# Kernel tuning notes

Hardware: AMD Instinct MI355X
Metric: run time of the kernel (lower is better)

## Reference

```python
import jax, jax.numpy as jnp
import numpy as np

N, E, G = 100_000, 1_200_000, 256
EPS = 1e-5

def _bn(a, g, b):
    # BatchNorm1d in training mode: biased batch statistics over dim 0
    mu = a.mean(0)
    var = ((a - mu) ** 2).mean(0)
    return (a - mu) * jax.lax.rsqrt(var + EPS) * g + b

def _cgconv(x, src, dst, ea, Wf, bf, Ws, bs, g, b):
    # PyG CGConv: z = [x_i, x_j, edge_attr]; m = sigmoid(lin_f(z)) * softplus(lin_s(z));
    # out = BN(scatter_add(m -> dst)) + x
    z = jnp.concatenate([x[dst], x[src], ea], axis=-1)      # [E, 2*64+1]
    m = jax.nn.sigmoid(z @ Wf + bf) * jax.nn.softplus(z @ Ws + bs)  # [E, 64]
    agg = jax.ops.segment_sum(m, dst, num_segments=x.shape[0])
    return _bn(agg, g, b) + x

def setup_inputs() -> dict:
    key = jax.random.key(0)
    ks = jax.random.split(key, 16)
    def w(k, shape, scale):
        return jax.random.normal(k, shape, jnp.float32) * scale
    inp = {
        "x": jax.random.normal(ks[0], (N, 12), jnp.float32),
        "edge_index": jax.random.randint(ks[1], (2, E), 0, N, jnp.int32),
        "edge_attr": jax.random.uniform(ks[2], (E, 1), dtype=jnp.float32),
        "batch": jnp.sort(jax.random.randint(ks[3], (N,), 0, G, jnp.int32)),
        "W_in": w(ks[4], (12, 64), 0.3), "b_in": jnp.zeros((64,), jnp.float32),
        "g0": jnp.ones((64,), jnp.float32), "beta0": jnp.zeros((64,), jnp.float32),
    }
    i = 5
    for l in (1, 2, 3):
        inp[f"Wf{l}"] = w(ks[i], (129, 64), 0.1)
        inp[f"bf{l}"] = jnp.zeros((64,), jnp.float32)
        inp[f"Ws{l}"] = w(ks[i + 1], (129, 64), 0.1)
        inp[f"bs{l}"] = jnp.zeros((64,), jnp.float32)
        inp[f"g{l}"] = jnp.ones((64,), jnp.float32)
        inp[f"bb{l}"] = jnp.zeros((64,), jnp.float32)
        i += 2
    inp["W1"] = w(ks[11], (64, 32), 0.15)
    inp["b1"] = jnp.zeros((32,), jnp.float32)
    inp["W2"] = w(ks[12], (32, 1), 0.2)
    inp["b2"] = jnp.zeros((1,), jnp.float32)
    return inp

def reference(x, edge_index, edge_attr, batch,
              W_in, b_in, g0, beta0,
              Wf1, bf1, Ws1, bs1, g1, bb1,
              Wf2, bf2, Ws2, bs2, g2, bb2,
              Wf3, bf3, Ws3, bs3, g3, bb3,
              W1, b1, W2, b2):
    src, dst = edge_index[0], edge_index[1]
    h = jax.nn.relu(_bn(x @ W_in + b_in, g0, beta0))
    h = jax.nn.relu(_cgconv(h, src, dst, edge_attr, Wf1, bf1, Ws1, bs1, g1, bb1))
    h = jax.nn.relu(_cgconv(h, src, dst, edge_attr, Wf2, bf2, Ws2, bs2, g2, bb2))
    h = _cgconv(h, src, dst, edge_attr, Wf3, bf3, Ws3, bs3, g3, bb3)
    # global_mean_pool
    s = jax.ops.segment_sum(h, batch, num_segments=G)
    c = jax.ops.segment_sum(jnp.ones((h.shape[0],), h.dtype), batch, num_segments=G)
    pooled = s / jnp.maximum(c, 1.0)[:, None]
    return jax.nn.relu(pooled @ W1 + b1) @ W2 + b2  # [G, 1]
```

## Files before the change

kernel.cpp:

```cpp
#include <hip/hip_runtime.h>
#include <math.h>

#define N_NODES 100000
#define N_EDGES 1200000
#define N_GRAPHS 256
#define CH 64
#define NC (N_NODES * CH)
#define EPS 1e-5f
#define LOG2E 1.4426950408889634f
#define LN2 0.6931471805599453f
#define EA_SCALE 32768.0f

#define ZSTRN 72
#define GTILES ((N_NODES + 63) / 64)
#define EA_BLOCKS 4096
#define NW (EA_BLOCKS * 4)
#define POOL_BLOCKS 256
#define WP2ROWS 64
#define CAP 48
#define LDSQ 1024

#define NCOLORS 8
#define SC_BLOCKS 2048
#define NCHUNK (SC_BLOCKS / NCOLORS)
#define CSZ ((N_EDGES + NCHUNK - 1) / NCHUNK)
#define RNODES ((N_NODES + NCOLORS - 1) / NCOLORS)

#define EMB_BLOCKS 512
#define PREP_BLOCKS 192
#define PRE_BLOCKS (SC_BLOCKS + EMB_BLOCKS + PREP_BLOCKS)

typedef _Float16 half8 __attribute__((ext_vector_type(8)));
typedef _Float16 half2v __attribute__((ext_vector_type(2)));
typedef float floatx4 __attribute__((ext_vector_type(4)));

__device__ __forceinline__ float gate2(float f2, float s2) {
    float ef = __builtin_amdgcn_exp2f(-f2);
    float sig = __builtin_amdgcn_rcpf(1.0f + ef);
    float es = __builtin_amdgcn_exp2f(-fabsf(s2));
    float sp = fmaxf(s2, 0.0f) + __builtin_amdgcn_logf(1.0f + es);
    return sig * sp;
}

__global__ void pre_kernel(const int* __restrict__ ei,
                           const float* __restrict__ ea,
                           int* __restrict__ cnt,
                           unsigned* __restrict__ sef2,
                           const float* __restrict__ x,
                           const float* __restrict__ W,
                           const float* __restrict__ b,
                           _Float16* __restrict__ emb,
                           float* __restrict__ stats,
                           const float* __restrict__ Wf0, const float* __restrict__ Ws0,
                           const float* __restrict__ bf0, const float* __restrict__ bs0,
                           const float* __restrict__ Wf1, const float* __restrict__ Ws1,
                           const float* __restrict__ bf1, const float* __restrict__ bs1,
                           const float* __restrict__ Wf2, const float* __restrict__ Ws2,
                           const float* __restrict__ bf2, const float* __restrict__ bs2,
                           _Float16* __restrict__ WT2,
                           float* __restrict__ w128,
                           float* __restrict__ bias) {
    __shared__ int lcnt;
    __shared__ int ldst[LDSQ];
    __shared__ unsigned lpay[LDSQ];
    const int bid = blockIdx.x;
    if (bid < SC_BLOCKS) {
        if (threadIdx.x == 0) lcnt = 0;
        __syncthreads();
        const int j = bid & (NCOLORS - 1);
        const int k = bid >> 3;
        const int dlo = j * RNODES;
        const int dhi = min(N_NODES, dlo + RNODES);
        const int e0 = k * CSZ;
        const int e1 = min(N_EDGES, e0 + CSZ);
        for (int e = e0 + threadIdx.x; e < e1; e += 256) {
            int d = ei[N_EDGES + e];
            if (d >= dlo && d < dhi) {
                unsigned v = ((unsigned)ei[e] << 15) | (unsigned)(ea[e] * EA_SCALE);
                int i = atomicAdd(&lcnt, 1);
                if (i < LDSQ) { ldst[i] = d; lpay[i] = v; }
                else {
                    int slot = atomicAdd(&cnt[d], 1);
                    if (slot < CAP) sef2[(size_t)d * CAP + slot] = v;
                }
            }
        }
        __syncthreads();
        const int m = min(lcnt, LDSQ);
        for (int i = threadIdx.x; i < m; i += 256) {
            int d = ldst[i];
            int slot = atomicAdd(&cnt[d], 1);
            if (slot < CAP) sef2[(size_t)d * CAP + slot] = lpay[i];
        }
    } else if (bid < SC_BLOCKS + EMB_BLOCKS) {
        const int eb = bid - SC_BLOCKS;
        int c = threadIdx.x & 63;
        int sub = threadIdx.x >> 6;
        float s = 0.f, q = 0.f;
        for (int r = eb * 4 + sub; r < N_NODES; r += EMB_BLOCKS * 4) {
            const float* xr = x + r * 12;
            float acc = b[c];
#pragma unroll
            for (int k = 0; k < 12; ++k)
                acc = fmaf(xr[k], W[k * CH + c], acc);
            _Float16 h = (_Float16)acc;
            emb[(size_t)r * CH + c] = h;
            float hf = (float)h;
            s += hf;
            q = fmaf(hf, hf, q);
        }
        __shared__ float ls[4][64];
        __shared__ float lq[4][64];
        ls[sub][c] = s;
        lq[sub][c] = q;
        __syncthreads();
        if (sub == 0) {
            s = ls[0][c] + ls[1][c] + ls[2][c] + ls[3][c];
            q = lq[0][c] + lq[1][c] + lq[2][c] + lq[3][c];
            atomicAdd(&stats[c], s);
            atomicAdd(&stats[64 + c], q);
        }
    } else {
        int gid = (bid - SC_BLOCKS - EMB_BLOCKS) * 256 + threadIdx.x;
        int l = gid >> 14;
        int idx = gid & 16383;
        if (l >= 3) return;
        const float* Wf = (l == 0) ? Wf0 : (l == 1) ? Wf1 : Wf2;
        const float* Ws = (l == 0) ? Ws0 : (l == 1) ? Ws1 : Ws2;
        const float* bf = (l == 0) ? bf0 : (l == 1) ? bf1 : bf2;
        const float* bs = (l == 0) ? bs0 : (l == 1) ? bs1 : bs2;
        {
            int cc = idx >> 6;
            int k = idx & 63;
            float v;
            if (cc < 128) {
                int ch = cc >> 1;
                v = (cc & 1) ? Ws[k * 64 + ch] : Wf[k * 64 + ch];
            } else {
                int jj = cc - 128, ch = jj >> 1;
                v = (jj & 1) ? Ws[(64 + k) * 64 + ch] : Wf[(64 + k) * 64 + ch];
            }
            WT2[l * 16384 + idx] = (_Float16)(v * LOG2E);
        }
        if (idx < 128) {
            w128[l * 128 + idx] = ((idx < 64) ? Wf[128 * 64 + idx] : Ws[128 * 64 + (idx - 64)])
                                  * (LOG2E / EA_SCALE);
            bias[l * 128 + idx] = ((idx < 64) ? bf[idx] : bs[idx - 64]) * LOG2E;
        }
    }
}

template <bool RES, bool RED>
__global__ __launch_bounds__(256)
void node_gemm_kernel(const _Float16* __restrict__ ain,
                      const _Float16* __restrict__ res,
                      const float* __restrict__ stats,
                      const float* __restrict__ gamma,
                      const float* __restrict__ beta,
                      const _Float16* __restrict__ WT2,
                      _Float16* __restrict__ hout,
                      _Float16* __restrict__ pqrs) {
    __shared__ __align__(16) _Float16 As[64 * ZSTRN];
    __shared__ __align__(16) float ab[128];
    __shared__ float sw[128];
    const int t = threadIdx.x;
    const int lane = t & 63;
    const int w = t >> 6;
    const int l15 = lane & 15;
    const int quad = lane >> 4;

    if (RED) {
        if (t < 128) {
            float s = 0.f;
#pragma unroll 8
            for (int r = 0; r < WP2ROWS; ++r) s += stats[r * 128 + t];
            sw[t] = s;
        }
        __syncthreads();
    }
    if (t < 64) {
        float s0 = RED ? sw[t] : stats[t];
        float s1 = RED ? sw[64 + t] : stats[64 + t];
        float mean = s0 * (1.0f / (float)N_NODES);
        float var  = s1 * (1.0f / (float)N_NODES) - mean * mean;
        float inv  = rsqrtf(var + EPS);
        float A = gamma[t] * inv;
        ab[t] = A;
        ab[64 + t] = beta[t] - mean * A;
    }

    half8 bfr[4][2];
#pragma unroll
    for (int tt = 0; tt < 4; ++tt)
#pragma unroll
        for (int ks = 0; ks < 2; ++ks)
            bfr[tt][ks] = *(const half8*)(WT2 + (w * 64 + tt * 16 + l15) * 64 + ks * 32 + quad * 8);
    __syncthreads();

    const int base = blockIdx.x * 64;
    {
        const int e = t >> 2, q = t & 3;
        const int row = base + e;
        const bool valid = (row < N_NODES);
        const int crow = valid ? row : (N_NODES - 1);
        float af[16];
        {
            const _Float16* aph = ain + (size_t)crow * CH + q * 16;
            half8 h0 = *(const half8*)aph;
            half8 h1 = *(const half8*)(aph + 8);
#pragma unroll
            for (int j = 0; j < 8; ++j) { af[j] = (float)h0[j]; af[8 + j] = (float)h1[j]; }
        }
        float rf[16];
        if (RES) {
            const _Float16* rph = res + (size_t)crow * CH + q * 16;
            half8 r0 = *(const half8*)rph;
            half8 r1 = *(const half8*)(rph + 8);
#pragma unroll
            for (int j = 0; j < 8; ++j) { rf[j] = (float)r0[j]; rf[8 + j] = (float)r1[j]; }
        }
        float vv[16];
#pragma unroll
        for (int i = 0; i < 4; ++i) {
            float4 A4 = *(const float4*)(ab + q * 16 + i * 4);
            float4 B4 = *(const float4*)(ab + 64 + q * 16 + i * 4);
#pragma unroll
            for (int jj = 0; jj < 4; ++jj) {
                float Ax = (jj == 0) ? A4.x : (jj == 1) ? A4.y : (jj == 2) ? A4.z : A4.w;
                float Bx = (jj == 0) ? B4.x : (jj == 1) ? B4.y : (jj == 2) ? B4.z : B4.w;
                float r = RES ? rf[i * 4 + jj] : 0.f;
                vv[i * 4 + jj] = fmaxf(fmaf(af[i * 4 + jj], Ax, Bx) + r, 0.0f);
            }
        }
        half8 o0, o1;
#pragma unroll
        for (int j = 0; j < 8; ++j) { o0[j] = (_Float16)vv[j]; o1[j] = (_Float16)vv[8 + j]; }
        *(half8*)(As + e * ZSTRN + q * 16) = o0;
        *(half8*)(As + e * ZSTRN + q * 16 + 8) = o1;
        if (valid) {
            half8* hp = (half8*)(hout + (size_t)row * CH + q * 16);
            hp[0] = o0;
            hp[1] = o1;
        }
    }
    __syncthreads();

    floatx4 acc[4][4];
#pragma unroll
    for (int rt = 0; rt < 4; ++rt)
#pragma unroll
        for (int tt = 0; tt < 4; ++tt)
#pragma unroll
            for (int r = 0; r < 4; ++r) acc[rt][tt][r] = 0.f;

#pragma unroll
    for (int ks = 0; ks < 2; ++ks) {
#pragma unroll
        for (int rt = 0; rt < 4; ++rt) {
            half8 a = *(const half8*)(As + (rt * 16 + l15) * ZSTRN + ks * 32 + quad * 8);
#pragma unroll
            for (int tt = 0; tt < 4; ++tt)
                acc[rt][tt] = __builtin_amdgcn_mfma_f32_16x16x32_f16(a, bfr[tt][ks], acc[rt][tt], 0, 0, 0);
        }
    }

#pragma unroll
    for (int rt = 0; rt < 4; ++rt) {
#pragma unroll
        for (int r = 0; r < 4; ++r) {
            int row = base + rt * 16 + quad * 4 + r;
            if (row < N_NODES) {
#pragma unroll
                for (int tt = 0; tt < 4; ++tt)
                    pqrs[(size_t)row * 256 + w * 64 + tt * 16 + l15] = (_Float16)acc[rt][tt][r];
            }
        }
    }
}

__global__ __launch_bounds__(256)
void edge_agg_kernel(const _Float16* __restrict__ pqrs,
                     const unsigned* __restrict__ sef2,
                     const int* __restrict__ cnt,
                     const float* __restrict__ w128,
                     const float* __restrict__ bias,
                     _Float16* __restrict__ agg,
                     float* __restrict__ wpart2) {
    const int lane = threadIdx.x & 63;
    const int w = threadIdx.x >> 6;
    const int gw = __builtin_amdgcn_readfirstlane(blockIdx.x * 4 + w);
    const float wfc = w128[lane], wsc = w128[64 + lane];
    const float bfc = bias[lane], bsc = bias[64 + lane];
    const half2v* __restrict__ prb = (const half2v*)pqrs;
    const half2v* __restrict__ qsb = (const half2v*)pqrs + 64;

    const int n0 = (int)((long)gw * N_NODES / NW);
    const int n1 = (int)((long)(gw + 1) * N_NODES / NW);

    float ssum = 0.f, sqsum = 0.f;
    if (n0 < n1) {
        half2v prn = prb[(size_t)n0 * 128 + lane];
        for (int n = n0; n < n1; ++n) {
            int deg = cnt[n];
            if (deg > CAP) deg = CAP;
            const unsigned* sp = sef2 + (size_t)n * CAP;
            half2v pr = prn;
            {
                int np = (n + 1 < N_NODES) ? (n + 1) : (N_NODES - 1);
                prn = prb[(size_t)np * 128 + lane];
            }
            const float fb = (float)pr[0] + bfc;
            const float sb = (float)pr[1] + bsc;
            float acc0 = 0.f, acc1 = 0.f, acc2 = 0.f, acc3 = 0.f;
            int e = 0;
            for (; e + 8 <= deg; e += 8) {
                unsigned s0 = sp[e],     s1 = sp[e + 1], s2 = sp[e + 2], s3 = sp[e + 3];
                unsigned s4 = sp[e + 4], s5 = sp[e + 5], s6 = sp[e + 6], s7 = sp[e + 7];
                half2v q0 = qsb[(size_t)(s0 >> 15) * 128 + lane];
                half2v q1 = qsb[(size_t)(s1 >> 15) * 128 + lane];
                half2v q2 = qsb[(size_t)(s2 >> 15) * 128 + lane];
                half2v q3 = qsb[(size_t)(s3 >> 15) * 128 + lane];
                half2v q4 = qsb[(size_t)(s4 >> 15) * 128 + lane];
                half2v q5 = qsb[(size_t)(s5 >> 15) * 128 + lane];
                half2v q6 = qsb[(size_t)(s6 >> 15) * 128 + lane];
                half2v q7 = qsb[(size_t)(s7 >> 15) * 128 + lane];
                float ea0 = (float)(s0 & 32767u), ea1 = (float)(s1 & 32767u);
                float ea2 = (float)(s2 & 32767u), ea3 = (float)(s3 & 32767u);
                float ea4 = (float)(s4 & 32767u), ea5 = (float)(s5 & 32767u);
                float ea6 = (float)(s6 & 32767u), ea7 = (float)(s7 & 32767u);
                acc0 += gate2(fmaf(ea0, wfc, fb + (float)q0[0]), fmaf(ea0, wsc, sb + (float)q0[1]));
                acc1 += gate2(fmaf(ea1, wfc, fb + (float)q1[0]), fmaf(ea1, wsc, sb + (float)q1[1]));
                acc2 += gate2(fmaf(ea2, wfc, fb + (float)q2[0]), fmaf(ea2, wsc, sb + (float)q2[1]));
                acc3 += gate2(fmaf(ea3, wfc, fb + (float)q3[0]), fmaf(ea3, wsc, sb + (float)q3[1]));
                acc0 += gate2(fmaf(ea4, wfc, fb + (float)q4[0]), fmaf(ea4, wsc, sb + (float)q4[1]));
                acc1 += gate2(fmaf(ea5, wfc, fb + (float)q5[0]), fmaf(ea5, wsc, sb + (float)q5[1]));
                acc2 += gate2(fmaf(ea6, wfc, fb + (float)q6[0]), fmaf(ea6, wsc, sb + (float)q6[1]));
                acc3 += gate2(fmaf(ea7, wfc, fb + (float)q7[0]), fmaf(ea7, wsc, sb + (float)q7[1]));
            }
            if (e + 4 <= deg) {
                unsigned s0 = sp[e], s1 = sp[e + 1], s2 = sp[e + 2], s3 = sp[e + 3];
                half2v q0 = qsb[(size_t)(s0 >> 15) * 128 + lane];
                half2v q1 = qsb[(size_t)(s1 >> 15) * 128 + lane];
                half2v q2 = qsb[(size_t)(s2 >> 15) * 128 + lane];
                half2v q3 = qsb[(size_t)(s3 >> 15) * 128 + lane];
                float ea0 = (float)(s0 & 32767u), ea1 = (float)(s1 & 32767u);
                float ea2 = (float)(s2 & 32767u), ea3 = (float)(s3 & 32767u);
                acc0 += gate2(fmaf(ea0, wfc, fb + (float)q0[0]), fmaf(ea0, wsc, sb + (float)q0[1]));
                acc1 += gate2(fmaf(ea1, wfc, fb + (float)q1[0]), fmaf(ea1, wsc, sb + (float)q1[1]));
                acc2 += gate2(fmaf(ea2, wfc, fb + (float)q2[0]), fmaf(ea2, wsc, sb + (float)q2[1]));
                acc3 += gate2(fmaf(ea3, wfc, fb + (float)q3[0]), fmaf(ea3, wsc, sb + (float)q3[1]));
                e += 4;
            }
            for (; e < deg; ++e) {
                unsigned s0 = sp[e];
                half2v q0 = qsb[(size_t)(s0 >> 15) * 128 + lane];
                float ea0 = (float)(s0 & 32767u);
                acc0 += gate2(fmaf(ea0, wfc, fb + (float)q0[0]), fmaf(ea0, wsc, sb + (float)q0[1]));
            }
            _Float16 ah = (_Float16)(LN2 * ((acc0 + acc1) + (acc2 + acc3)));
            agg[(size_t)n * CH + lane] = ah;
            float acc = (float)ah;
            ssum += acc;
            sqsum = fmaf(acc, acc, sqsum);
        }
    }
    __shared__ float reds[4][128];
    reds[w][lane] = ssum;
    reds[w][64 + lane] = sqsum;
    __syncthreads();
    if (w == 0) {
        float a = reds[0][lane] + reds[1][lane] + reds[2][lane] + reds[3][lane];
        float b = reds[0][64 + lane] + reds[1][64 + lane] + reds[2][64 + lane] + reds[3][64 + lane];
        float* wp = wpart2 + (size_t)(blockIdx.x & (WP2ROWS - 1)) * 128;
        atomicAdd(&wp[lane], a);
        atomicAdd(&wp[64 + lane], b);
    }
}

__global__ __launch_bounds__(256)
void pool_bn_kernel(const _Float16* __restrict__ ain,
                    const _Float16* __restrict__ res,
                    const float* __restrict__ wp2,
                    const float* __restrict__ gamma,
                    const float* __restrict__ beta,
                    const int* __restrict__ batch,
                    float* __restrict__ pooled,
                    float* __restrict__ counts) {
    __shared__ float sw[128];
    __shared__ float ab[128];
    if (threadIdx.x < 128) {
        float s = 0.f;
#pragma unroll 8
        for (int r = 0; r < WP2ROWS; ++r) s += wp2[r * 128 + threadIdx.x];
        sw[threadIdx.x] = s;
    }
    __syncthreads();
    if (threadIdx.x < 64) {
        int t = threadIdx.x;
        float mean = sw[t] * (1.0f / (float)N_NODES);
        float var  = sw[64 + t] * (1.0f / (float)N_NODES) - mean * mean;
        float inv  = rsqrtf(var + EPS);
        float A = gamma[t] * inv;
        ab[t] = A;
        ab[64 + t] = beta[t] - mean * A;
    }
    __syncthreads();

    const int c = threadIdx.x & 63;
    const float A = ab[c], B = ab[64 + c];
    const int walker = blockIdx.x * 4 + (threadIdx.x >> 6);
    const int nwalk = POOL_BLOCKS * 4;
    const int chunk = (N_NODES + nwalk - 1) / nwalk;
    int r0 = walker * chunk;
    int r1 = min(N_NODES, r0 + chunk);
    if (r0 >= r1) return;

    int cur = batch[r0];
    float acc = 0.0f;
    int runlen = 0;
    for (int r = r0; r < r1; ++r) {
        int b = batch[r];
        if (b != cur) {
            atomicAdd(&pooled[cur * CH + c], acc);
            if (c == 0) atomicAdd(&counts[cur], (float)runlen);
            acc = 0.0f;
            runlen = 0;
            cur = b;
        }
        size_t idx = (size_t)r * CH + c;
        acc += fmaf((float)ain[idx], A, B) + (float)res[idx];
        ++runlen;
    }
    atomicAdd(&pooled[cur * CH + c], acc);
    if (c == 0) atomicAdd(&counts[cur], (float)runlen);
}

__global__ void head_kernel(const float* __restrict__ pooled,
                            const float* __restrict__ counts,
                            const float* __restrict__ W1,
                            const float* __restrict__ b1,
                            const float* __restrict__ W2,
                            const float* __restrict__ b2,
                            float* __restrict__ out) {
    int gph = blockIdx.x;
    int t = threadIdx.x;
    __shared__ float p[64];
    __shared__ float h1[32];
    float cnt = fmaxf(counts[gph], 1.0f);
    p[t] = pooled[gph * CH + t] / cnt;
    __syncthreads();
    if (t < 32) {
        float acc = b1[t];
#pragma unroll
        for (int c = 0; c < 64; ++c)
            acc = fmaf(p[c], W1[c * 32 + t], acc);
        h1[t] = fmaxf(acc, 0.0f);
    }
    __syncthreads();
    if (t == 0) {
        float acc = b2[0];
#pragma unroll
        for (int j = 0; j < 32; ++j)
            acc = fmaf(h1[j], W2[j], acc);
        out[gph] = acc;
    }
}

extern "C" void kernel_launch(void* const* d_in, const int* in_sizes, int n_in,
                              void* d_out, int out_size, void* d_ws, size_t ws_size,
                              hipStream_t stream) {
    const float* x     = (const float*)d_in[0];
    const int*   ei    = (const int*)d_in[1];
    const float* ea    = (const float*)d_in[2];
    const int*   batch = (const int*)d_in[3];
    const float* W_in  = (const float*)d_in[4];
    const float* b_in  = (const float*)d_in[5];
    const float* g0    = (const float*)d_in[6];
    const float* beta0 = (const float*)d_in[7];

    const float* Wf[3] = {(const float*)d_in[8],  (const float*)d_in[14], (const float*)d_in[20]};
    const float* bfv[3]= {(const float*)d_in[9],  (const float*)d_in[15], (const float*)d_in[21]};
    const float* Wsv[3]= {(const float*)d_in[10], (const float*)d_in[16], (const float*)d_in[22]};
    const float* bsv[3]= {(const float*)d_in[11], (const float*)d_in[17], (const float*)d_in[23]};
    const float* gm[3] = {(const float*)d_in[12], (const float*)d_in[18], (const float*)d_in[24]};
    const float* bb[3] = {(const float*)d_in[13], (const float*)d_in[19], (const float*)d_in[25]};

    const float* W1 = (const float*)d_in[26];
    const float* b1 = (const float*)d_in[27];
    const float* W2 = (const float*)d_in[28];
    const float* b2 = (const float*)d_in[29];

    float* out = (float*)d_out;

#define ALIGN256(v) (((v) + 255) & ~(size_t)255)
    char* base = (char*)d_ws;
    size_t off = 0;
    _Float16* bufA = (_Float16*)(base + off); off = ALIGN256(off + (size_t)NC * 2);
    _Float16* bufB = (_Float16*)(base + off); off = ALIGN256(off + (size_t)NC * 2);
    _Float16* AGG = (_Float16*)(base + off);  off = ALIGN256(off + (size_t)NC * 2);
    _Float16* WT2 = (_Float16*)(base + off);  off = ALIGN256(off + 3 * 256 * 64 * 2);
    float* w128   = (float*)(base + off);     off = ALIGN256(off + 3 * 128 * 4);
    float* biasL  = (float*)(base + off);     off = ALIGN256(off + 3 * 128 * 4);
    unsigned* sef2 = (unsigned*)(base + off); off = ALIGN256(off + (size_t)N_NODES * CAP * 4);
    _Float16* pqrs = (_Float16*)(base + off); off = ALIGN256(off + (size_t)N_NODES * 256 * 2);
    char* zbase   = base + off;
    int* cnt      = (int*)(base + off);       off = ALIGN256(off + (size_t)N_NODES * 4);
    float* stats0 = (float*)(base + off);     off = ALIGN256(off + 128 * 4);
    float* wpart2 = (float*)(base + off);     off = ALIGN256(off + 3 * WP2ROWS * 128 * 4);
    float* pooled = (float*)(base + off);     off = ALIGN256(off + (size_t)N_GRAPHS * CH * 4);
    float* counts = (float*)(base + off);     off = ALIGN256(off + (size_t)N_GRAPHS * 4);
    size_t zbytes = (size_t)(base + off - zbase);

    hipMemsetAsync(zbase, 0, zbytes, stream);

    pre_kernel<<<PRE_BLOCKS, 256, 0, stream>>>(
        ei, ea, cnt, sef2, x, W_in, b_in, bufA, stats0,
        Wf[0], Wsv[0], bfv[0], bsv[0],
        Wf[1], Wsv[1], bfv[1], bsv[1],
        Wf[2], Wsv[2], bfv[2], bsv[2],
        WT2, w128, biasL);

    node_gemm_kernel<false, false><<<GTILES, 256, 0, stream>>>(
        bufA, nullptr, stats0, g0, beta0, WT2 + 0 * 256 * 64, bufB, pqrs);
    edge_agg_kernel<<<EA_BLOCKS, 256, 0, stream>>>(
        pqrs, sef2, cnt, w128 + 0 * 128, biasL + 0 * 128, AGG,
        wpart2 + 0 * WP2ROWS * 128);

    node_gemm_kernel<true, true><<<GTILES, 256, 0, stream>>>(
        AGG, bufB, wpart2 + 0 * WP2ROWS * 128, gm[0], bb[0], WT2 + 1 * 256 * 64, bufA, pqrs);
    edge_agg_kernel<<<EA_BLOCKS, 256, 0, stream>>>(
        pqrs, sef2, cnt, w128 + 1 * 128, biasL + 1 * 128, AGG,
        wpart2 + 1 * WP2ROWS * 128);

    node_gemm_kernel<true, true><<<GTILES, 256, 0, stream>>>(
        AGG, bufA, wpart2 + 1 * WP2ROWS * 128, gm[1], bb[1], WT2 + 2 * 256 * 64, bufB, pqrs);
    edge_agg_kernel<<<EA_BLOCKS, 256, 0, stream>>>(
        pqrs, sef2, cnt, w128 + 2 * 128, biasL + 2 * 128, AGG,
        wpart2 + 2 * WP2ROWS * 128);

    pool_bn_kernel<<<POOL_BLOCKS, 256, 0, stream>>>(
        AGG, bufB, wpart2 + 2 * WP2ROWS * 128, gm[2], bb[2], batch, pooled, counts);
    head_kernel<<<N_GRAPHS, 64, 0, stream>>>(pooled, counts, W1, b1, W2, b2, out);
}
```

Baseline: 499.0 us.

## Move edge scatter into first node GEMM kernel to overlap with GEMM

The edge bucketing scatter (building per-destination edge lists) moves out of the pre kernel and into a new combined kernel. There its blocks are interleaved with the first-layer node GEMM tiles, so the memory- and atomic-bound scatter runs alongside the MFMA-bound GEMM. The pre kernel now only does the embedding and weight preparation, so it is shorter and the GEMM no longer waits for the scatter. The trade-off is higher LDS use per block in the combined kernel, which may lower occupancy for the GEMM blocks.

```diff
diff --git a/kernel.cpp b/kernel.cpp
--- a/kernel.cpp
+++ b/kernel.cpp
@@ -28,7 +28,12 @@
 
 #define EMB_BLOCKS 512
 #define PREP_BLOCKS 192
-#define PRE_BLOCKS (SC_BLOCKS + EMB_BLOCKS + PREP_BLOCKS)
+#define PRE2_BLOCKS (EMB_BLOCKS + PREP_BLOCKS)
+
+#define GS_GROUPS 196
+#define GS_ILV (GS_GROUPS * 16)
+#define GS_SCAT_ILV (GS_GROUPS * 8)
+#define GS_BLOCKS (GS_ILV + (SC_BLOCKS - GS_SCAT_ILV))
 
 typedef _Float16 half8 __attribute__((ext_vector_type(8)));
 typedef _Float16 half2v __attribute__((ext_vector_type(2)));
@@ -42,62 +47,26 @@
     return sig * sp;
 }
 
-__global__ void pre_kernel(const int* __restrict__ ei,
-                           const float* __restrict__ ea,
-                           int* __restrict__ cnt,
-                           unsigned* __restrict__ sef2,
-                           const float* __restrict__ x,
-                           const float* __restrict__ W,
-                           const float* __restrict__ b,
-                           _Float16* __restrict__ emb,
-                           float* __restrict__ stats,
-                           const float* __restrict__ Wf0, const float* __restrict__ Ws0,
-                           const float* __restrict__ bf0, const float* __restrict__ bs0,
-                           const float* __restrict__ Wf1, const float* __restrict__ Ws1,
-                           const float* __restrict__ bf1, const float* __restrict__ bs1,
-                           const float* __restrict__ Wf2, const float* __restrict__ Ws2,
-                           const float* __restrict__ bf2, const float* __restrict__ bs2,
-                           _Float16* __restrict__ WT2,
-                           float* __restrict__ w128,
-                           float* __restrict__ bias) {
-    __shared__ int lcnt;
-    __shared__ int ldst[LDSQ];
-    __shared__ unsigned lpay[LDSQ];
+__global__ void pre2_kernel(const float* __restrict__ x,
+                            const float* __restrict__ W,
+                            const float* __restrict__ b,
+                            _Float16* __restrict__ emb,
+                            float* __restrict__ stats,
+                            const float* __restrict__ Wf0, const float* __restrict__ Ws0,
+                            const float* __restrict__ bf0, const float* __restrict__ bs0,
+                            const float* __restrict__ Wf1, const float* __restrict__ Ws1,
+                            const float* __restrict__ bf1, const float* __restrict__ bs1,
+                            const float* __restrict__ Wf2, const float* __restrict__ Ws2,
+                            const float* __restrict__ bf2, const float* __restrict__ bs2,
+                            _Float16* __restrict__ WT2,
+                            float* __restrict__ w128,
+                            float* __restrict__ bias) {
     const int bid = blockIdx.x;
-    if (bid < SC_BLOCKS) {
-        if (threadIdx.x == 0) lcnt = 0;
-        __syncthreads();
-        const int j = bid & (NCOLORS - 1);
-        const int k = bid >> 3;
-        const int dlo = j * RNODES;
-        const int dhi = min(N_NODES, dlo + RNODES);
-        const int e0 = k * CSZ;
-        const int e1 = min(N_EDGES, e0 + CSZ);
-        for (int e = e0 + threadIdx.x; e < e1; e += 256) {
-            int d = ei[N_EDGES + e];
-            if (d >= dlo && d < dhi) {
-                unsigned v = ((unsigned)ei[e] << 15) | (unsigned)(ea[e] * EA_SCALE);
-                int i = atomicAdd(&lcnt, 1);
-                if (i < LDSQ) { ldst[i] = d; lpay[i] = v; }
-                else {
-                    int slot = atomicAdd(&cnt[d], 1);
-                    if (slot < CAP) sef2[(size_t)d * CAP + slot] = v;
-                }
-            }
-        }
-        __syncthreads();
-        const int m = min(lcnt, LDSQ);
-        for (int i = threadIdx.x; i < m; i += 256) {
-            int d = ldst[i];
-            int slot = atomicAdd(&cnt[d], 1);
-            if (slot < CAP) sef2[(size_t)d * CAP + slot] = lpay[i];
-        }
-    } else if (bid < SC_BLOCKS + EMB_BLOCKS) {
-        const int eb = bid - SC_BLOCKS;
+    if (bid < EMB_BLOCKS) {
         int c = threadIdx.x & 63;
         int sub = threadIdx.x >> 6;
         float s = 0.f, q = 0.f;
-        for (int r = eb * 4 + sub; r < N_NODES; r += EMB_BLOCKS * 4) {
+        for (int r = bid * 4 + sub; r < N_NODES; r += EMB_BLOCKS * 4) {
             const float* xr = x + r * 12;
             float acc = b[c];
 #pragma unroll
@@ -121,7 +90,7 @@
             atomicAdd(&stats[64 + c], q);
         }
     } else {
-        int gid = (bid - SC_BLOCKS - EMB_BLOCKS) * 256 + threadIdx.x;
+        int gid = (bid - EMB_BLOCKS) * 256 + threadIdx.x;
         int l = gid >> 14;
         int idx = gid & 16383;
         if (l >= 3) return;
@@ -146,6 +115,160 @@
             w128[l * 128 + idx] = ((idx < 64) ? Wf[128 * 64 + idx] : Ws[128 * 64 + (idx - 64)])
                                   * (LOG2E / EA_SCALE);
             bias[l * 128 + idx] = ((idx < 64) ? bf[idx] : bs[idx - 64]) * LOG2E;
+        }
+    }
+}
+
+__global__ __launch_bounds__(256)
+void gemm0_scatter_kernel(const int* __restrict__ ei,
+                          const float* __restrict__ ea,
+                          int* __restrict__ cnt,
+                          unsigned* __restrict__ sef2,
+                          const _Float16* __restrict__ ain,
+                          const float* __restrict__ stats,
+                          const float* __restrict__ gamma,
+                          const float* __restrict__ beta,
+                          const _Float16* __restrict__ WT2,
+                          _Float16* __restrict__ hout,
+                          _Float16* __restrict__ pqrs) {
+    __shared__ __align__(16) _Float16 As[64 * ZSTRN];
+    __shared__ __align__(16) float ab[128];
+    __shared__ int lcnt;
+    __shared__ int ldst[LDSQ];
+    __shared__ unsigned lpay[LDSQ];
+
+    const int bid = blockIdx.x;
+    int gemm_tile = -1, scat_id = -1;
+    if (bid < GS_ILV) {
+        int g = bid >> 4, sub = bid & 15;
+        if (sub < 8) { gemm_tile = g * 8 + sub; if (gemm_tile >= GTILES) return; }
+        else scat_id = g * 8 + (sub - 8);
+    } else {
+        scat_id = GS_SCAT_ILV + (bid - GS_ILV);
+    }
+
+    if (scat_id >= 0) {
+        if (threadIdx.x == 0) lcnt = 0;
+        __syncthreads();
+        const int j = scat_id & (NCOLORS - 1);
+        const int k = scat_id >> 3;
+        const int dlo = j * RNODES;
+        const int dhi = min(N_NODES, dlo + RNODES);
+        const int e0 = k * CSZ;
+        const int e1 = min(N_EDGES, e0 + CSZ);
+        for (int e = e0 + threadIdx.x; e < e1; e += 256) {
+            int d = ei[N_EDGES + e];
+            if (d >= dlo && d < dhi) {
+                unsigned v = ((unsigned)ei[e] << 15) | (unsigned)(ea[e] * EA_SCALE);
+                int i = atomicAdd(&lcnt, 1);
+                if (i < LDSQ) { ldst[i] = d; lpay[i] = v; }
+                else {
+                    int slot = atomicAdd(&cnt[d], 1);
+                    if (slot < CAP) sef2[(size_t)d * CAP + slot] = v;
+                }
+            }
+        }
+        __syncthreads();
+        const int m = min(lcnt, LDSQ);
+        for (int i = threadIdx.x; i < m; i += 256) {
+            int d = ldst[i];
+            int slot = atomicAdd(&cnt[d], 1);
+            if (slot < CAP) sef2[(size_t)d * CAP + slot] = lpay[i];
+        }
+        return;
+    }
+
+    const int t = threadIdx.x;
+    const int lane = t & 63;
+    const int w = t >> 6;
+    const int l15 = lane & 15;
+    const int quad = lane >> 4;
+
+    if (t < 64) {
+        float mean = stats[t] * (1.0f / (float)N_NODES);
+        float var  = stats[64 + t] * (1.0f / (float)N_NODES) - mean * mean;
+        float inv  = rsqrtf(var + EPS);
+        float A = gamma[t] * inv;
+        ab[t] = A;
+        ab[64 + t] = beta[t] - mean * A;
+    }
+
+    half8 bfr[4][2];
+#pragma unroll
+    for (int tt = 0; tt < 4; ++tt)
+#pragma unroll
+        for (int ks = 0; ks < 2; ++ks)
+            bfr[tt][ks] = *(const half8*)(WT2 + (w * 64 + tt * 16 + l15) * 64 + ks * 32 + quad * 8);
+    __syncthreads();
+
+    const int base = gemm_tile * 64;
+    {
+        const int e = t >> 2, q = t & 3;
+        const int row = base + e;
+        const bool valid = (row < N_NODES);
+        const int crow = valid ? row : (N_NODES - 1);
+        float af[16];
+        {
+            const _Float16* aph = ain + (size_t)crow * CH + q * 16;
+            half8 h0 = *(const half8*)aph;
+            half8 h1 = *(const half8*)(aph + 8);
+#pragma unroll
+            for (int jj = 0; jj < 8; ++jj) { af[jj] = (float)h0[jj]; af[8 + jj] = (float)h1[jj]; }
+        }
+        float vv[16];
+#pragma unroll
+        for (int i = 0; i < 4; ++i) {
+            float4 A4 = *(const float4*)(ab + q * 16 + i * 4);
+            float4 B4 = *(const float4*)(ab + 64 + q * 16 + i * 4);
+#pragma unroll
+            for (int jj = 0; jj < 4; ++jj) {
+                float Ax = (jj == 0) ? A4.x : (jj == 1) ? A4.y : (jj == 2) ? A4.z : A4.w;
+                float Bx = (jj == 0) ? B4.x : (jj == 1) ? B4.y : (jj == 2) ? B4.z : B4.w;
+                vv[i * 4 + jj] = fmaxf(fmaf(af[i * 4 + jj], Ax, Bx), 0.0f);
+            }
+        }
+        half8 o0, o1;
+#pragma unroll
+        for (int jj = 0; jj < 8; ++jj) { o0[jj] = (_Float16)vv[jj]; o1[jj] = (_Float16)vv[8 + jj]; }
+        *(half8*)(As + e * ZSTRN + q * 16) = o0;
+        *(half8*)(As + e * ZSTRN + q * 16 + 8) = o1;
+        if (valid) {
+            half8* hp = (half8*)(hout + (size_t)row * CH + q * 16);
+            hp[0] = o0;
+            hp[1] = o1;
+        }
+    }
+    __syncthreads();
+
+    floatx4 acc[4][4];
+#pragma unroll
+    for (int rt = 0; rt < 4; ++rt)
+#pragma unroll
+        for (int tt = 0; tt < 4; ++tt)
+#pragma unroll
+            for (int r = 0; r < 4; ++r) acc[rt][tt][r] = 0.f;
+
+#pragma unroll
+    for (int ks = 0; ks < 2; ++ks) {
+#pragma unroll
+        for (int rt = 0; rt < 4; ++rt) {
+            half8 a = *(const half8*)(As + (rt * 16 + l15) * ZSTRN + ks * 32 + quad * 8);
+#pragma unroll
+            for (int tt = 0; tt < 4; ++tt)
+                acc[rt][tt] = __builtin_amdgcn_mfma_f32_16x16x32_f16(a, bfr[tt][ks], acc[rt][tt], 0, 0, 0);
+        }
+    }
+
+#pragma unroll
+    for (int rt = 0; rt < 4; ++rt) {
+#pragma unroll
+        for (int r = 0; r < 4; ++r) {
+            int row = base + rt * 16 + quad * 4 + r;
+            if (row < N_NODES) {
+#pragma unroll
+                for (int tt = 0; tt < 4; ++tt)
+                    pqrs[(size_t)row * 256 + w * 64 + tt * 16 + l15] = (_Float16)acc[rt][tt][r];
+            }
         }
     }
 }
@@ -513,15 +636,17 @@
 
     hipMemsetAsync(zbase, 0, zbytes, stream);
 
-    pre_kernel<<<PRE_BLOCKS, 256, 0, stream>>>(
-        ei, ea, cnt, sef2, x, W_in, b_in, bufA, stats0,
+    pre2_kernel<<<PRE2_BLOCKS, 256, 0, stream>>>(
+        x, W_in, b_in, bufA, stats0,
         Wf[0], Wsv[0], bfv[0], bsv[0],
         Wf[1], Wsv[1], bfv[1], bsv[1],
         Wf[2], Wsv[2], bfv[2], bsv[2],
         WT2, w128, biasL);
 
-    node_gemm_kernel<false, false><<<GTILES, 256, 0, stream>>>(
-        bufA, nullptr, stats0, g0, beta0, WT2 + 0 * 256 * 64, bufB, pqrs);
+    gemm0_scatter_kernel<<<GS_BLOCKS, 256, 0, stream>>>(
+        ei, ea, cnt, sef2,
+        bufA, stats0, g0, beta0, WT2 + 0 * 256 * 64, bufB, pqrs);
+
     edge_agg_kernel<<<EA_BLOCKS, 256, 0, stream>>>(
         pqrs, sef2, cnt, w128 + 0 * 128, biasL + 0 * 128, AGG,
         wpart2 + 0 * WP2ROWS * 128);
```

Result: slower. 521.8 us (+4.6%).

## Partition edge bucketing by node range with LDS per-node counters

Applied to the files above, without the earlier changes.

The edge-to-destination bucketing now uses 32 blocks, each owning a contiguous range of about 3125 destination nodes. Each block scans the whole destination array with vectorized int4 loads and uses shared-memory atomics for per-node slot counts, instead of global atomics on cnt. Counts are written back once per node, so cnt no longer needs to be zeroed by the memset. The cost is that every block reads all 1.2M destinations, and only 32 blocks do the scatter, which may leave much of the GPU idle and lengthen the critical path of the pre kernel.

```diff
diff --git a/kernel.cpp b/kernel.cpp
--- a/kernel.cpp
+++ b/kernel.cpp
@@ -18,17 +18,13 @@
 #define POOL_BLOCKS 256
 #define WP2ROWS 64
 #define CAP 48
-#define LDSQ 1024
-
-#define NCOLORS 8
-#define SC_BLOCKS 2048
-#define NCHUNK (SC_BLOCKS / NCOLORS)
-#define CSZ ((N_EDGES + NCHUNK - 1) / NCHUNK)
-#define RNODES ((N_NODES + NCOLORS - 1) / NCOLORS)
+
+#define SCAT_BLOCKS 32
+#define SRN ((N_NODES + SCAT_BLOCKS - 1) / SCAT_BLOCKS)
 
 #define EMB_BLOCKS 512
 #define PREP_BLOCKS 192
-#define PRE_BLOCKS (SC_BLOCKS + EMB_BLOCKS + PREP_BLOCKS)
+#define PRE3_BLOCKS (SCAT_BLOCKS + EMB_BLOCKS + PREP_BLOCKS)
 
 typedef _Float16 half8 __attribute__((ext_vector_type(8)));
 typedef _Float16 half2v __attribute__((ext_vector_type(2)));
@@ -42,58 +38,78 @@
     return sig * sp;
 }
 
-__global__ void pre_kernel(const int* __restrict__ ei,
-                           const float* __restrict__ ea,
-                           int* __restrict__ cnt,
-                           unsigned* __restrict__ sef2,
-                           const float* __restrict__ x,
-                           const float* __restrict__ W,
-                           const float* __restrict__ b,
-                           _Float16* __restrict__ emb,
-                           float* __restrict__ stats,
-                           const float* __restrict__ Wf0, const float* __restrict__ Ws0,
-                           const float* __restrict__ bf0, const float* __restrict__ bs0,
-                           const float* __restrict__ Wf1, const float* __restrict__ Ws1,
-                           const float* __restrict__ bf1, const float* __restrict__ bs1,
-                           const float* __restrict__ Wf2, const float* __restrict__ Ws2,
-                           const float* __restrict__ bf2, const float* __restrict__ bs2,
-                           _Float16* __restrict__ WT2,
-                           float* __restrict__ w128,
-                           float* __restrict__ bias) {
-    __shared__ int lcnt;
-    __shared__ int ldst[LDSQ];
-    __shared__ unsigned lpay[LDSQ];
+__global__ __launch_bounds__(256)
+void pre3_kernel(const int* __restrict__ ei,
+                 const float* __restrict__ ea,
+                 int* __restrict__ cnt,
+                 unsigned* __restrict__ sef2,
+                 const float* __restrict__ x,
+                 const float* __restrict__ W,
+                 const float* __restrict__ b,
+                 _Float16* __restrict__ emb,
+                 float* __restrict__ stats,
+                 const float* __restrict__ Wf0, const float* __restrict__ Ws0,
+                 const float* __restrict__ bf0, const float* __restrict__ bs0,
+                 const float* __restrict__ Wf1, const float* __restrict__ Ws1,
+                 const float* __restrict__ bf1, const float* __restrict__ bs1,
+                 const float* __restrict__ Wf2, const float* __restrict__ Ws2,
+                 const float* __restrict__ bf2, const float* __restrict__ bs2,
+                 _Float16* __restrict__ WT2,
+                 float* __restrict__ w128,
+                 float* __restrict__ bias) {
+    __shared__ int lcnt[SRN];
     const int bid = blockIdx.x;
-    if (bid < SC_BLOCKS) {
-        if (threadIdx.x == 0) lcnt = 0;
+    if (bid < SCAT_BLOCKS) {
+        const int nlo = bid * SRN;
+        const int nhi = min(N_NODES, nlo + SRN);
+        const int nr = nhi - nlo;
+        for (int i = threadIdx.x; i < nr; i += 256) lcnt[i] = 0;
         __syncthreads();
-        const int j = bid & (NCOLORS - 1);
-        const int k = bid >> 3;
-        const int dlo = j * RNODES;
-        const int dhi = min(N_NODES, dlo + RNODES);
-        const int e0 = k * CSZ;
-        const int e1 = min(N_EDGES, e0 + CSZ);
-        for (int e = e0 + threadIdx.x; e < e1; e += 256) {
-            int d = ei[N_EDGES + e];
-            if (d >= dlo && d < dhi) {
-                unsigned v = ((unsigned)ei[e] << 15) | (unsigned)(ea[e] * EA_SCALE);
-                int i = atomicAdd(&lcnt, 1);
-                if (i < LDSQ) { ldst[i] = d; lpay[i] = v; }
-                else {
-                    int slot = atomicAdd(&cnt[d], 1);
-                    if (slot < CAP) sef2[(size_t)d * CAP + slot] = v;
-                }
-            }
-        }
+
+        const int4* dstv = (const int4*)(ei + N_EDGES);
+        const int NV = N_EDGES / 4;
+
+#define PROC1(dd, ee) \
+        if ((dd) >= nlo && (dd) < nhi) { \
+            int slot = atomicAdd(&lcnt[(dd) - nlo], 1); \
+            if (slot < CAP) { \
+                unsigned val = ((unsigned)ei[ee] << 15) | (unsigned)(ea[ee] * EA_SCALE); \
+                sef2[(size_t)(dd) * CAP + slot] = val; \
+            } \
+        }
+#define PROC4(d4, eb) \
+        PROC1((d4).x, (eb)) PROC1((d4).y, (eb) + 1) \
+        PROC1((d4).z, (eb) + 2) PROC1((d4).w, (eb) + 3)
+
+        int v = threadIdx.x;
+        for (; v + 7 * 256 < NV; v += 8 * 256) {
+            int4 d0 = dstv[v];
+            int4 d1 = dstv[v + 256];
+            int4 d2 = dstv[v + 2 * 256];
+            int4 d3 = dstv[v + 3 * 256];
+            int4 d4 = dstv[v + 4 * 256];
+            int4 d5 = dstv[v + 5 * 256];
+            int4 d6 = dstv[v + 6 * 256];
+            int4 d7 = dstv[v + 7 * 256];
+            PROC4(d0, v * 4)
+            PROC4(d1, (v + 256) * 4)
+            PROC4(d2, (v + 2 * 256) * 4)
+            PROC4(d3, (v + 3 * 256) * 4)
+            PROC4(d4, (v + 4 * 256) * 4)
+            PROC4(d5, (v + 5 * 256) * 4)
+            PROC4(d6, (v + 6 * 256) * 4)
+            PROC4(d7, (v + 7 * 256) * 4)
+        }
+        for (; v < NV; v += 256) {
+            int4 d = dstv[v];
+            PROC4(d, v * 4)
+        }
+#undef PROC4
+#undef PROC1
         __syncthreads();
-        const int m = min(lcnt, LDSQ);
-        for (int i = threadIdx.x; i < m; i += 256) {
-            int d = ldst[i];
-            int slot = atomicAdd(&cnt[d], 1);
-            if (slot < CAP) sef2[(size_t)d * CAP + slot] = lpay[i];
-        }
-    } else if (bid < SC_BLOCKS + EMB_BLOCKS) {
-        const int eb = bid - SC_BLOCKS;
+        for (int i = threadIdx.x; i < nr; i += 256) cnt[nlo + i] = lcnt[i];
+    } else if (bid < SCAT_BLOCKS + EMB_BLOCKS) {
+        const int eb = bid - SCAT_BLOCKS;
         int c = threadIdx.x & 63;
         int sub = threadIdx.x >> 6;
         float s = 0.f, q = 0.f;
@@ -121,7 +137,7 @@
             atomicAdd(&stats[64 + c], q);
         }
     } else {
-        int gid = (bid - SC_BLOCKS - EMB_BLOCKS) * 256 + threadIdx.x;
+        int gid = (bid - SCAT_BLOCKS - EMB_BLOCKS) * 256 + threadIdx.x;
         int l = gid >> 14;
         int idx = gid & 16383;
         if (l >= 3) return;
@@ -503,8 +519,8 @@
     float* biasL  = (float*)(base + off);     off = ALIGN256(off + 3 * 128 * 4);
     unsigned* sef2 = (unsigned*)(base + off); off = ALIGN256(off + (size_t)N_NODES * CAP * 4);
     _Float16* pqrs = (_Float16*)(base + off); off = ALIGN256(off + (size_t)N_NODES * 256 * 2);
+    int* cnt      = (int*)(base + off);       off = ALIGN256(off + (size_t)N_NODES * 4);
     char* zbase   = base + off;
-    int* cnt      = (int*)(base + off);       off = ALIGN256(off + (size_t)N_NODES * 4);
     float* stats0 = (float*)(base + off);     off = ALIGN256(off + 128 * 4);
     float* wpart2 = (float*)(base + off);     off = ALIGN256(off + 3 * WP2ROWS * 128 * 4);
     float* pooled = (float*)(base + off);     off = ALIGN256(off + (size_t)N_GRAPHS * CH * 4);
@@ -513,7 +529,7 @@
 
     hipMemsetAsync(zbase, 0, zbytes, stream);
 
-    pre_kernel<<<PRE_BLOCKS, 256, 0, stream>>>(
+    pre3_kernel<<<PRE3_BLOCKS, 256, 0, stream>>>(
         ei, ea, cnt, sef2, x, W_in, b_in, bufA, stats0,
         Wf[0], Wsv[0], bfv[0], bsv[0],
         Wf[1], Wsv[1], bfv[1], bsv[1],
```

New measurement: 1.722 ms. 3.45x slower.
